# Performance work log

Hardware: AMD Instinct MI355X
Metric: run time of the kernel (lower is better)

Reference implementation:

```python
import jax, jax.numpy as jnp
import numpy as np

N_NODES = 200000
N_EDGES = 600000
FP = 128


def _gru_cell(x, h, wih, whh, bih, bhh):
    # torch.nn.GRUCell: gates ordered (r, z, n)
    gi = x @ wih.T + bih
    gh = h @ whh.T + bhh
    ir, iz, inn = jnp.split(gi, 3, axis=-1)
    hr, hz, hn = jnp.split(gh, 3, axis=-1)
    r = jax.nn.sigmoid(ir + hr)
    z = jax.nn.sigmoid(iz + hz)
    n = jnp.tanh(inn + r * hn)
    return (1.0 - z) * n + z * h


def _layer(x, dst, step, aw, ab, tw, tb, wih, whh, bih, bhh):
    n_nodes = x.shape[0]
    x_i = x[dst]  # [E, F] gather of target-node features
    if step == 0:
        h_s = jnp.broadcast_to(jnp.sum(x_i, axis=-1, keepdims=True), x_i.shape)
    else:
        h_s = x_i
    esv = jax.nn.leaky_relu(jnp.concatenate([h_s, x_i], axis=-1) @ aw.T + ab)  # [E,1]
    asv = jax.nn.softmax(esv, axis=-1)  # size-1 softmax -> ones (faithful)
    cs = jax.nn.elu(asv * (h_s @ tw.T + tb))  # dropout is identity at eval
    m = _gru_cell(cs, h_s, wih, whh, bih, bhh)  # per-edge GRU update [E,F]
    return jax.ops.segment_sum(m, dst, num_segments=n_nodes)  # scatter-add aggregate


def setup_inputs() -> dict:
    key = jax.random.key(0)
    ks = jax.random.split(key, 20)
    s = 1.0 / np.sqrt(FP)
    inp = {
        "x": jax.random.normal(ks[0], (N_NODES, FP), dtype=jnp.float32),
        "edge_index": jax.random.randint(ks[1], (2, N_EDGES), 0, N_NODES, dtype=jnp.int64),
    }
    i = 2
    for l in range(2):
        inp[f"align_w{l}"] = jax.random.uniform(ks[i], (1, 2 * FP), jnp.float32, -s, s); i += 1
        inp[f"align_b{l}"] = jax.random.uniform(ks[i], (1,), jnp.float32, -s, s); i += 1
        inp[f"attend_w{l}"] = jax.random.uniform(ks[i], (FP, FP), jnp.float32, -s, s); i += 1
        inp[f"attend_b{l}"] = jax.random.uniform(ks[i], (FP,), jnp.float32, -s, s); i += 1
        inp[f"wih{l}"] = jax.random.uniform(ks[i], (3 * FP, FP), jnp.float32, -s, s); i += 1
        inp[f"whh{l}"] = jax.random.uniform(ks[i], (3 * FP, FP), jnp.float32, -s, s); i += 1
        inp[f"bih{l}"] = jax.random.uniform(ks[i], (3 * FP,), jnp.float32, -s, s); i += 1
        inp[f"bhh{l}"] = jax.random.uniform(ks[i], (3 * FP,), jnp.float32, -s, s); i += 1
    return inp


def reference(x, edge_index,
              align_w0, align_b0, attend_w0, attend_b0, wih0, whh0, bih0, bhh0,
              align_w1, align_b1, attend_w1, attend_b1, wih1, whh1, bih1, bhh1):
    dst = edge_index[1]
    x = _layer(x, dst, 0, align_w0, align_b0, attend_w0, attend_b0, wih0, whh0, bih0, bhh0)
    x = _layer(x, dst, 1, align_w1, align_b1, attend_w1, attend_b1, wih1, whh1, bih1, bhh1)
    return x
```

## Files before the change

### kernel.cpp

```cpp
#include <hip/hip_runtime.h>
#include <cmath>

#define NN 200000
#define NE 600000

typedef __bf16 bf16x8 __attribute__((ext_vector_type(8)));
typedef float f32x4 __attribute__((ext_vector_type(4)));

#define LOG2E 1.44269504088896340736f
__device__ __forceinline__ float fexp2(float x) { return __builtin_amdgcn_exp2f(x); }
__device__ __forceinline__ float frcp(float x) { return __builtin_amdgcn_rcpf(x); }
__device__ __forceinline__ float sigm(float v) { return frcp(1.0f + fexp2(-LOG2E * v)); }
__device__ __forceinline__ float ftanh(float v) {
  float t = fexp2(-2.0f * LOG2E * fabsf(v));
  float r = (1.0f - t) * frcp(1.0f + t);
  return __builtin_copysignf(r, v);
}
__device__ __forceinline__ float eluf(float v) { return v > 0.0f ? v : fexp2(LOG2E * v) - 1.0f; }

__device__ __forceinline__ unsigned short bfr(float f) {
  unsigned u = __float_as_uint(f);
  u += 0x7FFFu + ((u >> 16) & 1u);
  return (unsigned short)(u >> 16);
}
__device__ __forceinline__ void bsplit(float v, unsigned short& hi, unsigned short& lo) {
  unsigned short h = bfr(v);
  float hf = __uint_as_float(((unsigned)h) << 16);
  hi = h;
  lo = bfr(v - hf);
}


__global__ __launch_bounds__(256) void hist_kernel(const int* __restrict__ dst,
                                                   int* __restrict__ deg) {
  int e = blockIdx.x * 256 + threadIdx.x;
  if (e < NE) atomicAdd(&deg[dst[e]], 1);
}

__global__ __launch_bounds__(512) void prep_kernel(const float* __restrict__ attw0,
                                                   const float* __restrict__ whh0,
                                                   float* __restrict__ rwt0,
                                                   float* __restrict__ rwh0) {
  int t = threadIdx.x;
  if (t < 128) {
    float s = 0.f;
    for (int k = 0; k < 128; k++) s += attw0[t * 128 + k];
    rwt0[t] = s;
  } else {
    int j = t - 128;
    float s = 0.f;
    for (int k = 0; k < 128; k++) s += whh0[j * 128 + k];
    rwh0[j] = s;
  }
}

__global__ __launch_bounds__(256) void pack_kernel(
    const float* __restrict__ wih0, const float* __restrict__ tw1,
    const float* __restrict__ wih1, const float* __restrict__ whh1,
    unsigned short* __restrict__ w0ph, unsigned short* __restrict__ w0pl,
    unsigned short* __restrict__ w1ph, unsigned short* __restrict__ w1pl,
    unsigned short* __restrict__ w2ph, unsigned short* __restrict__ w2pl) {
  int g = blockIdx.x * 256 + threadIdx.x;
  unsigned short *PH, *PL;
  const float* row;
  int l;
  if (g < 6144) { l = g; PH = w0ph; PL = w0pl; }
  else if (g < 8192) { l = g - 6144; PH = w1ph; PL = w1pl; }
  else if (g < 20480) { l = g - 8192; PH = w2ph; PL = w2pl; }
  else return;
  int lane = l & 63, ks = (l >> 6) & 3, nt = l >> 8;
  int n = nt * 16 + (lane & 15);
  int k0 = ks * 32 + (lane >> 4) * 8;
  if (g < 6144) row = wih0 + n * 128;
  else if (g < 8192) row = tw1 + n * 128;
  else row = (n < 384) ? wih1 + n * 128 : whh1 + (n - 384) * 128;
  unsigned uh[4], ul[4];
  for (int p = 0; p < 4; p++) {
    unsigned short ah, al, bh, bl;
    bsplit(row[k0 + 2 * p], ah, al);
    bsplit(row[k0 + 2 * p + 1], bh, bl);
    uh[p] = (unsigned)ah | ((unsigned)bh << 16);
    ul[p] = (unsigned)al | ((unsigned)bl << 16);
  }
  *(uint4*)&PH[l * 8] = make_uint4(uh[0], uh[1], uh[2], uh[3]);
  *(uint4*)&PL[l * 8] = make_uint4(ul[0], ul[1], ul[2], ul[3]);
}

#define MFMA3(accv, ah, al, bh, bl)                                          \
  accv = __builtin_amdgcn_mfma_f32_16x16x32_bf16(ah, bh, accv, 0, 0, 0);     \
  accv = __builtin_amdgcn_mfma_f32_16x16x32_bf16(ah, bl, accv, 0, 0, 0);     \
  accv = __builtin_amdgcn_mfma_f32_16x16x32_bf16(al, bh, accv, 0, 0, 0);

__global__ __launch_bounds__(256, 2) void layer0_kernel(
    const float* __restrict__ x, const float* __restrict__ tb0,
    const unsigned short* __restrict__ w0ph, const unsigned short* __restrict__ w0pl,
    const float* __restrict__ bih0, const float* __restrict__ bhh0,
    const float* __restrict__ rwt0, const float* __restrict__ rwh0,
    const int* __restrict__ deg, float* __restrict__ x1) {
  __shared__ float s_lds[32];
  __shared__ float deg_lds[32];
  __shared__ unsigned short csh[32 * 136];
  __shared__ unsigned short csl[32 * 136];

  const int tid = threadIdx.x;
  const int lane = tid & 63;
  const int wv = tid >> 6;
  const int n0 = blockIdx.x * 32;

  if (tid < 32) deg_lds[tid] = (float)deg[n0 + tid];

  {
    int m = tid >> 3, c = (tid & 7) * 16;
    const float4* xr = (const float4*)(x + (size_t)(n0 + m) * 128 + c);
    float a = 0.f;
#pragma unroll
    for (int q = 0; q < 4; q++) { float4 v = xr[q]; a += v.x + v.y + v.z + v.w; }
#pragma unroll
    for (int o = 1; o < 8; o <<= 1) a += __shfl_xor(a, o, 64);
    if ((tid & 7) == 0) s_lds[m] = a;
  }
  __syncthreads();

  {
    int m = tid >> 3, c0 = (tid & 7) * 16;
    float s = s_lds[m];
#pragma unroll
    for (int q = 0; q < 4; q++) {
      int k = c0 + q * 4;
      unsigned short h0, l0, h1, l1, h2, l2, h3, l3;
      bsplit(eluf(fmaf(s, rwt0[k], tb0[k])), h0, l0);
      bsplit(eluf(fmaf(s, rwt0[k + 1], tb0[k + 1])), h1, l1);
      bsplit(eluf(fmaf(s, rwt0[k + 2], tb0[k + 2])), h2, l2);
      bsplit(eluf(fmaf(s, rwt0[k + 3], tb0[k + 3])), h3, l3);
      *(uint2*)&csh[m * 136 + k] =
          make_uint2((unsigned)h0 | ((unsigned)h1 << 16), (unsigned)h2 | ((unsigned)h3 << 16));
      *(uint2*)&csl[m * 136 + k] =
          make_uint2((unsigned)l0 | ((unsigned)l1 << 16), (unsigned)l2 | ((unsigned)l3 << 16));
    }
  }
  __syncthreads();

  const int mrow = lane & 15;
  const int kq = (lane >> 4) * 8;
  const int quad = lane >> 4;
  f32x4 acc[2][2][3] = {};
#pragma unroll
  for (int ks = 0; ks < 4; ks++) {
    bf16x8 a0h = *(const bf16x8*)&csh[mrow * 136 + ks * 32 + kq];
    bf16x8 a0l = *(const bf16x8*)&csl[mrow * 136 + ks * 32 + kq];
    bf16x8 a1h = *(const bf16x8*)&csh[(16 + mrow) * 136 + ks * 32 + kq];
    bf16x8 a1l = *(const bf16x8*)&csl[(16 + mrow) * 136 + ks * 32 + kq];
#pragma unroll
    for (int jj = 0; jj < 2; jj++) {
      int jt = wv + jj * 4;
#pragma unroll
      for (int g = 0; g < 3; g++) {
        int nt = g * 8 + jt;
        size_t base = (size_t)((nt * 4 + ks) * 64 + lane) * 8;
        bf16x8 bh = *(const bf16x8*)&w0ph[base];
        bf16x8 bl = *(const bf16x8*)&w0pl[base];
        MFMA3(acc[0][jj][g], a0h, a0l, bh, bl);
        MFMA3(acc[1][jj][g], a1h, a1l, bh, bl);
      }
    }
  }

  float bir[2], biz[2], bin_[2], bhr[2], bhz[2], bhn[2], rwr[2], rwz[2], rwn[2];
#pragma unroll
  for (int jj = 0; jj < 2; jj++) {
    int j = (wv + jj * 4) * 16 + mrow;
    bir[jj] = bih0[j]; biz[jj] = bih0[j + 128]; bin_[jj] = bih0[j + 256];
    bhr[jj] = bhh0[j]; bhz[jj] = bhh0[j + 128]; bhn[jj] = bhh0[j + 256];
    rwr[jj] = rwh0[j]; rwz[jj] = rwh0[j + 128]; rwn[jj] = rwh0[j + 256];
  }
#pragma unroll
  for (int mt = 0; mt < 2; mt++) {
#pragma unroll
    for (int reg = 0; reg < 4; reg++) {
      int m = mt * 16 + quad * 4 + reg;
      float s = s_lds[m];
      float dd = deg_lds[m];
#pragma unroll
      for (int jj = 0; jj < 2; jj++) {
        float gir = acc[mt][jj][0][reg] + bir[jj];
        float giz = acc[mt][jj][1][reg] + biz[jj];
        float gin = acc[mt][jj][2][reg] + bin_[jj];
        float ghr = fmaf(s, rwr[jj], bhr[jj]);
        float ghz = fmaf(s, rwz[jj], bhz[jj]);
        float ghn = fmaf(s, rwn[jj], bhn[jj]);
        float r = sigm(gir + ghr);
        float z = sigm(giz + ghz);
        float nn = ftanh(fmaf(r, ghn, gin));
        int j = (wv + jj * 4) * 16 + mrow;
        x1[(size_t)(n0 + m) * 128 + j] = dd * ((1.f - z) * nn + z * s);
      }
    }
  }
}

__global__ __launch_bounds__(256, 2) void layer1_kernel(
    const float* __restrict__ x1, const float* __restrict__ tb1,
    const unsigned short* __restrict__ w1ph, const unsigned short* __restrict__ w1pl,
    const unsigned short* __restrict__ w2ph, const unsigned short* __restrict__ w2pl,
    const float* __restrict__ bih1, const float* __restrict__ bhh1,
    const int* __restrict__ deg, float* __restrict__ out) {
  __shared__ unsigned short hh[32 * 136];
  __shared__ unsigned short hl[32 * 136];
  __shared__ unsigned short ch[32 * 136];
  __shared__ unsigned short cl[32 * 136];
  __shared__ float deg_lds[32];

  const int tid = threadIdx.x;
  const int lane = tid & 63;
  const int wv = tid >> 6;
  const int n0 = blockIdx.x * 32;
  const int mrow = lane & 15;
  const int kq = (lane >> 4) * 8;
  const int quad = lane >> 4;

  if (tid < 32) deg_lds[tid] = (float)deg[n0 + tid];

  {
    int m = tid >> 3, c0 = (tid & 7) * 16;
    const float4* xr = (const float4*)(x1 + (size_t)(n0 + m) * 128 + c0);
#pragma unroll
    for (int q = 0; q < 4; q++) {
      float4 v = xr[q];
      unsigned short h0, l0, h1, l1, h2, l2, h3, l3;
      bsplit(v.x, h0, l0); bsplit(v.y, h1, l1);
      bsplit(v.z, h2, l2); bsplit(v.w, h3, l3);
      *(uint2*)&hh[m * 136 + c0 + q * 4] =
          make_uint2((unsigned)h0 | ((unsigned)h1 << 16), (unsigned)h2 | ((unsigned)h3 << 16));
      *(uint2*)&hl[m * 136 + c0 + q * 4] =
          make_uint2((unsigned)l0 | ((unsigned)l1 << 16), (unsigned)l2 | ((unsigned)l3 << 16));
    }
  }
  __syncthreads();

  f32x4 acc1[2][2] = {};
#pragma unroll
  for (int ks = 0; ks < 4; ks++) {
    bf16x8 a0h = *(const bf16x8*)&hh[mrow * 136 + ks * 32 + kq];
    bf16x8 a0l = *(const bf16x8*)&hl[mrow * 136 + ks * 32 + kq];
    bf16x8 a1h = *(const bf16x8*)&hh[(16 + mrow) * 136 + ks * 32 + kq];
    bf16x8 a1l = *(const bf16x8*)&hl[(16 + mrow) * 136 + ks * 32 + kq];
#pragma unroll
    for (int jj = 0; jj < 2; jj++) {
      int nt = wv + jj * 4;
      size_t base = (size_t)((nt * 4 + ks) * 64 + lane) * 8;
      bf16x8 bh = *(const bf16x8*)&w1ph[base];
      bf16x8 bl = *(const bf16x8*)&w1pl[base];
      MFMA3(acc1[0][jj], a0h, a0l, bh, bl);
      MFMA3(acc1[1][jj], a1h, a1l, bh, bl);
    }
  }
  {
    float tbj[2];
#pragma unroll
    for (int jj = 0; jj < 2; jj++) tbj[jj] = tb1[(wv + jj * 4) * 16 + mrow];
#pragma unroll
    for (int mt = 0; mt < 2; mt++)
#pragma unroll
      for (int jj = 0; jj < 2; jj++)
#pragma unroll
        for (int reg = 0; reg < 4; reg++) {
          int m = mt * 16 + quad * 4 + reg;
          unsigned short vh, vl;
          bsplit(eluf(acc1[mt][jj][reg] + tbj[jj]), vh, vl);
          unsigned pv = (unsigned)vh | ((unsigned)vl << 16);
          unsigned pu = __shfl_xor(pv, 1, 64);
          if ((lane & 1) == 0) {
            int j = (wv + jj * 4) * 16 + mrow;
            unsigned hpack = (pv & 0xFFFFu) | (pu << 16);
            unsigned lpack = (pv >> 16) | (pu & 0xFFFF0000u);
            *(unsigned*)&ch[m * 136 + j] = hpack;
            *(unsigned*)&cl[m * 136 + j] = lpack;
          }
        }
  }
  __syncthreads();

  f32x4 acc2[2][2][6] = {};
#pragma unroll
  for (int ks = 0; ks < 4; ks++) {
    bf16x8 c0h = *(const bf16x8*)&ch[mrow * 136 + ks * 32 + kq];
    bf16x8 c0l = *(const bf16x8*)&cl[mrow * 136 + ks * 32 + kq];
    bf16x8 c1h = *(const bf16x8*)&ch[(16 + mrow) * 136 + ks * 32 + kq];
    bf16x8 c1l = *(const bf16x8*)&cl[(16 + mrow) * 136 + ks * 32 + kq];
    bf16x8 x0h = *(const bf16x8*)&hh[mrow * 136 + ks * 32 + kq];
    bf16x8 x0l = *(const bf16x8*)&hl[mrow * 136 + ks * 32 + kq];
    bf16x8 x1h = *(const bf16x8*)&hh[(16 + mrow) * 136 + ks * 32 + kq];
    bf16x8 x1l = *(const bf16x8*)&hl[(16 + mrow) * 136 + ks * 32 + kq];
#pragma unroll
    for (int jj = 0; jj < 2; jj++) {
      int jt = wv + jj * 4;
#pragma unroll
      for (int g = 0; g < 3; g++) {
        int nt = g * 8 + jt;
        size_t base = (size_t)((nt * 4 + ks) * 64 + lane) * 8;
        bf16x8 bh = *(const bf16x8*)&w2ph[base];
        bf16x8 bl = *(const bf16x8*)&w2pl[base];
        MFMA3(acc2[0][jj][g], c0h, c0l, bh, bl);
        MFMA3(acc2[1][jj][g], c1h, c1l, bh, bl);
      }
#pragma unroll
      for (int g = 0; g < 3; g++) {
        int nt = 24 + g * 8 + jt;
        size_t base = (size_t)((nt * 4 + ks) * 64 + lane) * 8;
        bf16x8 bh = *(const bf16x8*)&w2ph[base];
        bf16x8 bl = *(const bf16x8*)&w2pl[base];
        MFMA3(acc2[0][jj][3 + g], x0h, x0l, bh, bl);
        MFMA3(acc2[1][jj][3 + g], x1h, x1l, bh, bl);
      }
    }
  }

  float bir[2], biz[2], bin_[2], bhr[2], bhz[2], bhn[2];
#pragma unroll
  for (int jj = 0; jj < 2; jj++) {
    int j = (wv + jj * 4) * 16 + mrow;
    bir[jj] = bih1[j]; biz[jj] = bih1[j + 128]; bin_[jj] = bih1[j + 256];
    bhr[jj] = bhh1[j]; bhz[jj] = bhh1[j + 128]; bhn[jj] = bhh1[j + 256];
  }
#pragma unroll
  for (int mt = 0; mt < 2; mt++) {
#pragma unroll
    for (int reg = 0; reg < 4; reg++) {
      int m = mt * 16 + quad * 4 + reg;
      float dd = deg_lds[m];
#pragma unroll
      for (int jj = 0; jj < 2; jj++) {
        int j = (wv + jj * 4) * 16 + mrow;
        float gir = acc2[mt][jj][0][reg] + bir[jj];
        float giz = acc2[mt][jj][1][reg] + biz[jj];
        float gin = acc2[mt][jj][2][reg] + bin_[jj];
        float ghr = acc2[mt][jj][3][reg] + bhr[jj];
        float ghz = acc2[mt][jj][4][reg] + bhz[jj];
        float ghn = acc2[mt][jj][5][reg] + bhn[jj];
        float r = sigm(gir + ghr);
        float z = sigm(giz + ghz);
        float nn = ftanh(fmaf(r, ghn, gin));
        float hfull = (float)(*(const __bf16*)&hh[m * 136 + j]) +
                      (float)(*(const __bf16*)&hl[m * 136 + j]);
        out[(size_t)(n0 + m) * 128 + j] = dd * ((1.f - z) * nn + z * hfull);
      }
    }
  }
}

extern "C" void kernel_launch(void* const* d_in, const int* in_sizes, int n_in,
                              void* d_out, int out_size, void* d_ws, size_t ws_size,
                              hipStream_t stream) {
  const float* x     = (const float*)d_in[0];
  const int*   edge  = (const int*)d_in[1];
  const float* attw0 = (const float*)d_in[4];
  const float* attb0 = (const float*)d_in[5];
  const float* wih0  = (const float*)d_in[6];
  const float* whh0  = (const float*)d_in[7];
  const float* bih0  = (const float*)d_in[8];
  const float* bhh0  = (const float*)d_in[9];
  const float* attw1 = (const float*)d_in[12];
  const float* attb1 = (const float*)d_in[13];
  const float* wih1  = (const float*)d_in[14];
  const float* whh1  = (const float*)d_in[15];
  const float* bih1  = (const float*)d_in[16];
  const float* bhh1  = (const float*)d_in[17];

  float* ws   = (float*)d_ws;
  float* x1   = ws;
  int*   deg  = (int*)(ws + 25600000);
  float* rwt0 = ws + 25800000;
  float* rwh0 = ws + 25800128;
  unsigned short* wp = (unsigned short*)(ws + 25800512);
  unsigned short* w0ph = wp;
  unsigned short* w0pl = wp + 49152;
  unsigned short* w1ph = wp + 98304;
  unsigned short* w1pl = wp + 114688;
  unsigned short* w2ph = wp + 131072;
  unsigned short* w2pl = wp + 229376;

  const int* dst = edge + NE;

  hipMemsetAsync(deg, 0, NN * sizeof(int), stream);
  hist_kernel<<<(NE + 255) / 256, 256, 0, stream>>>(dst, deg);
  prep_kernel<<<1, 512, 0, stream>>>(attw0, whh0, rwt0, rwh0);
  pack_kernel<<<80, 256, 0, stream>>>(wih0, attw1, wih1, whh1,
                                      w0ph, w0pl, w1ph, w1pl, w2ph, w2pl);
  layer0_kernel<<<NN / 32, 256, 0, stream>>>(x, attb0, w0ph, w0pl, bih0, bhh0,
                                             rwt0, rwh0, deg, x1);
  layer1_kernel<<<NN / 32, 256, 0, stream>>>(x1, attb1, w1ph, w1pl, w2ph, w2pl,
                                             bih1, bhh1, deg, (float*)d_out);
}
```

Before: 493.7 us.

## Use 64-node tiles with 8 waves each owning one output column tile

Both layer kernels now process 64 nodes per block with 512 threads. Each of the 8 waves owns a single 16-column output tile across four 16-row M tiles, so each weight fragment loaded from global is reused across four MFMA row tiles instead of two. Layer1 also interleaves the x-side GRU matmul with the attend matmul in the first K loop. It moves its LDS buffers to dynamic shared memory with a raised size limit. The cost is more accumulator registers per thread (24 f32x4 in layer1) and larger LDS use, which may lower occupancy.

```diff
diff --git a/kernel.cpp b/kernel.cpp
--- a/kernel.cpp
+++ b/kernel.cpp
@@ -91,23 +91,23 @@
   accv = __builtin_amdgcn_mfma_f32_16x16x32_bf16(ah, bl, accv, 0, 0, 0);     \
   accv = __builtin_amdgcn_mfma_f32_16x16x32_bf16(al, bh, accv, 0, 0, 0);
 
-__global__ __launch_bounds__(256, 2) void layer0_kernel(
+__global__ __launch_bounds__(512, 4) void layer0_kernel(
     const float* __restrict__ x, const float* __restrict__ tb0,
     const unsigned short* __restrict__ w0ph, const unsigned short* __restrict__ w0pl,
     const float* __restrict__ bih0, const float* __restrict__ bhh0,
     const float* __restrict__ rwt0, const float* __restrict__ rwh0,
     const int* __restrict__ deg, float* __restrict__ x1) {
-  __shared__ float s_lds[32];
-  __shared__ float deg_lds[32];
-  __shared__ unsigned short csh[32 * 136];
-  __shared__ unsigned short csl[32 * 136];
+  __shared__ float s_lds[64];
+  __shared__ float deg_lds[64];
+  __shared__ unsigned short csh[64 * 136];
+  __shared__ unsigned short csl[64 * 136];
 
   const int tid = threadIdx.x;
   const int lane = tid & 63;
   const int wv = tid >> 6;
-  const int n0 = blockIdx.x * 32;
-
-  if (tid < 32) deg_lds[tid] = (float)deg[n0 + tid];
+  const int n0 = blockIdx.x * 64;
+
+  if (tid < 64) deg_lds[tid] = (float)deg[n0 + tid];
 
   {
     int m = tid >> 3, c = (tid & 7) * 16;
@@ -143,82 +143,73 @@
   const int mrow = lane & 15;
   const int kq = (lane >> 4) * 8;
   const int quad = lane >> 4;
-  f32x4 acc[2][2][3] = {};
+  f32x4 acc[4][3] = {};
 #pragma unroll
   for (int ks = 0; ks < 4; ks++) {
-    bf16x8 a0h = *(const bf16x8*)&csh[mrow * 136 + ks * 32 + kq];
-    bf16x8 a0l = *(const bf16x8*)&csl[mrow * 136 + ks * 32 + kq];
-    bf16x8 a1h = *(const bf16x8*)&csh[(16 + mrow) * 136 + ks * 32 + kq];
-    bf16x8 a1l = *(const bf16x8*)&csl[(16 + mrow) * 136 + ks * 32 + kq];
-#pragma unroll
-    for (int jj = 0; jj < 2; jj++) {
-      int jt = wv + jj * 4;
-#pragma unroll
-      for (int g = 0; g < 3; g++) {
-        int nt = g * 8 + jt;
-        size_t base = (size_t)((nt * 4 + ks) * 64 + lane) * 8;
-        bf16x8 bh = *(const bf16x8*)&w0ph[base];
-        bf16x8 bl = *(const bf16x8*)&w0pl[base];
-        MFMA3(acc[0][jj][g], a0h, a0l, bh, bl);
-        MFMA3(acc[1][jj][g], a1h, a1l, bh, bl);
-      }
-    }
-  }
-
-  float bir[2], biz[2], bin_[2], bhr[2], bhz[2], bhn[2], rwr[2], rwz[2], rwn[2];
-#pragma unroll
-  for (int jj = 0; jj < 2; jj++) {
-    int j = (wv + jj * 4) * 16 + mrow;
-    bir[jj] = bih0[j]; biz[jj] = bih0[j + 128]; bin_[jj] = bih0[j + 256];
-    bhr[jj] = bhh0[j]; bhz[jj] = bhh0[j + 128]; bhn[jj] = bhh0[j + 256];
-    rwr[jj] = rwh0[j]; rwz[jj] = rwh0[j + 128]; rwn[jj] = rwh0[j + 256];
-  }
-#pragma unroll
-  for (int mt = 0; mt < 2; mt++) {
+    bf16x8 ah[4], al[4];
+#pragma unroll
+    for (int mt = 0; mt < 4; mt++) {
+      ah[mt] = *(const bf16x8*)&csh[(mt * 16 + mrow) * 136 + ks * 32 + kq];
+      al[mt] = *(const bf16x8*)&csl[(mt * 16 + mrow) * 136 + ks * 32 + kq];
+    }
+#pragma unroll
+    for (int g = 0; g < 3; g++) {
+      int nt = g * 8 + wv;
+      size_t base = (size_t)((nt * 4 + ks) * 64 + lane) * 8;
+      bf16x8 bh = *(const bf16x8*)&w0ph[base];
+      bf16x8 bl = *(const bf16x8*)&w0pl[base];
+#pragma unroll
+      for (int mt = 0; mt < 4; mt++) { MFMA3(acc[mt][g], ah[mt], al[mt], bh, bl); }
+    }
+  }
+
+  const int j = wv * 16 + mrow;
+  float bir = bih0[j], biz = bih0[j + 128], bin_ = bih0[j + 256];
+  float bhr = bhh0[j], bhz = bhh0[j + 128], bhn = bhh0[j + 256];
+  float rwr = rwh0[j], rwz = rwh0[j + 128], rwn = rwh0[j + 256];
+#pragma unroll
+  for (int mt = 0; mt < 4; mt++) {
 #pragma unroll
     for (int reg = 0; reg < 4; reg++) {
       int m = mt * 16 + quad * 4 + reg;
       float s = s_lds[m];
       float dd = deg_lds[m];
-#pragma unroll
-      for (int jj = 0; jj < 2; jj++) {
-        float gir = acc[mt][jj][0][reg] + bir[jj];
-        float giz = acc[mt][jj][1][reg] + biz[jj];
-        float gin = acc[mt][jj][2][reg] + bin_[jj];
-        float ghr = fmaf(s, rwr[jj], bhr[jj]);
-        float ghz = fmaf(s, rwz[jj], bhz[jj]);
-        float ghn = fmaf(s, rwn[jj], bhn[jj]);
-        float r = sigm(gir + ghr);
-        float z = sigm(giz + ghz);
-        float nn = ftanh(fmaf(r, ghn, gin));
-        int j = (wv + jj * 4) * 16 + mrow;
-        x1[(size_t)(n0 + m) * 128 + j] = dd * ((1.f - z) * nn + z * s);
-      }
-    }
-  }
-}
-
-__global__ __launch_bounds__(256, 2) void layer1_kernel(
+      float gir = acc[mt][0][reg] + bir;
+      float giz = acc[mt][1][reg] + biz;
+      float gin = acc[mt][2][reg] + bin_;
+      float ghr = fmaf(s, rwr, bhr);
+      float ghz = fmaf(s, rwz, bhz);
+      float ghn = fmaf(s, rwn, bhn);
+      float r = sigm(gir + ghr);
+      float z = sigm(giz + ghz);
+      float nn2 = ftanh(fmaf(r, ghn, gin));
+      x1[(size_t)(n0 + m) * 128 + j] = dd * ((1.f - z) * nn2 + z * s);
+    }
+  }
+}
+
+__global__ __launch_bounds__(512, 2) void layer1_kernel(
     const float* __restrict__ x1, const float* __restrict__ tb1,
     const unsigned short* __restrict__ w1ph, const unsigned short* __restrict__ w1pl,
     const unsigned short* __restrict__ w2ph, const unsigned short* __restrict__ w2pl,
     const float* __restrict__ bih1, const float* __restrict__ bhh1,
     const int* __restrict__ deg, float* __restrict__ out) {
-  __shared__ unsigned short hh[32 * 136];
-  __shared__ unsigned short hl[32 * 136];
-  __shared__ unsigned short ch[32 * 136];
-  __shared__ unsigned short cl[32 * 136];
-  __shared__ float deg_lds[32];
+  extern __shared__ unsigned short smem[];
+  unsigned short* hh = smem;
+  unsigned short* hl = smem + 8704;
+  unsigned short* ch = smem + 17408;
+  unsigned short* cl = smem + 26112;
+  __shared__ float deg_lds[64];
 
   const int tid = threadIdx.x;
   const int lane = tid & 63;
   const int wv = tid >> 6;
-  const int n0 = blockIdx.x * 32;
+  const int n0 = blockIdx.x * 64;
   const int mrow = lane & 15;
   const int kq = (lane >> 4) * 8;
   const int quad = lane >> 4;
 
-  if (tid < 32) deg_lds[tid] = (float)deg[n0 + tid];
+  if (tid < 64) deg_lds[tid] = (float)deg[n0 + tid];
 
   {
     int m = tid >> 3, c0 = (tid & 7) * 16;
@@ -237,113 +228,97 @@
   }
   __syncthreads();
 
-  f32x4 acc1[2][2] = {};
+  f32x4 acc1[4] = {};
+  f32x4 acc2[4][6] = {};
 #pragma unroll
   for (int ks = 0; ks < 4; ks++) {
-    bf16x8 a0h = *(const bf16x8*)&hh[mrow * 136 + ks * 32 + kq];
-    bf16x8 a0l = *(const bf16x8*)&hl[mrow * 136 + ks * 32 + kq];
-    bf16x8 a1h = *(const bf16x8*)&hh[(16 + mrow) * 136 + ks * 32 + kq];
-    bf16x8 a1l = *(const bf16x8*)&hl[(16 + mrow) * 136 + ks * 32 + kq];
-#pragma unroll
-    for (int jj = 0; jj < 2; jj++) {
-      int nt = wv + jj * 4;
-      size_t base = (size_t)((nt * 4 + ks) * 64 + lane) * 8;
+    bf16x8 xh[4], xl[4];
+#pragma unroll
+    for (int mt = 0; mt < 4; mt++) {
+      xh[mt] = *(const bf16x8*)&hh[(mt * 16 + mrow) * 136 + ks * 32 + kq];
+      xl[mt] = *(const bf16x8*)&hl[(mt * 16 + mrow) * 136 + ks * 32 + kq];
+    }
+    {
+      size_t base = (size_t)((wv * 4 + ks) * 64 + lane) * 8;
       bf16x8 bh = *(const bf16x8*)&w1ph[base];
       bf16x8 bl = *(const bf16x8*)&w1pl[base];
-      MFMA3(acc1[0][jj], a0h, a0l, bh, bl);
-      MFMA3(acc1[1][jj], a1h, a1l, bh, bl);
-    }
-  }
+#pragma unroll
+      for (int mt = 0; mt < 4; mt++) { MFMA3(acc1[mt], xh[mt], xl[mt], bh, bl); }
+    }
+#pragma unroll
+    for (int g = 0; g < 3; g++) {
+      int nt = 24 + g * 8 + wv;
+      size_t base = (size_t)((nt * 4 + ks) * 64 + lane) * 8;
+      bf16x8 bh = *(const bf16x8*)&w2ph[base];
+      bf16x8 bl = *(const bf16x8*)&w2pl[base];
+#pragma unroll
+      for (int mt = 0; mt < 4; mt++) { MFMA3(acc2[mt][3 + g], xh[mt], xl[mt], bh, bl); }
+    }
+  }
+
   {
-    float tbj[2];
-#pragma unroll
-    for (int jj = 0; jj < 2; jj++) tbj[jj] = tb1[(wv + jj * 4) * 16 + mrow];
-#pragma unroll
-    for (int mt = 0; mt < 2; mt++)
-#pragma unroll
-      for (int jj = 0; jj < 2; jj++)
-#pragma unroll
-        for (int reg = 0; reg < 4; reg++) {
-          int m = mt * 16 + quad * 4 + reg;
-          unsigned short vh, vl;
-          bsplit(eluf(acc1[mt][jj][reg] + tbj[jj]), vh, vl);
-          unsigned pv = (unsigned)vh | ((unsigned)vl << 16);
-          unsigned pu = __shfl_xor(pv, 1, 64);
-          if ((lane & 1) == 0) {
-            int j = (wv + jj * 4) * 16 + mrow;
-            unsigned hpack = (pv & 0xFFFFu) | (pu << 16);
-            unsigned lpack = (pv >> 16) | (pu & 0xFFFF0000u);
-            *(unsigned*)&ch[m * 136 + j] = hpack;
-            *(unsigned*)&cl[m * 136 + j] = lpack;
-          }
+    float tbj = tb1[wv * 16 + mrow];
+#pragma unroll
+    for (int mt = 0; mt < 4; mt++) {
+#pragma unroll
+      for (int reg = 0; reg < 4; reg++) {
+        int m = mt * 16 + quad * 4 + reg;
+        unsigned short vh, vl;
+        bsplit(eluf(acc1[mt][reg] + tbj), vh, vl);
+        unsigned pv = (unsigned)vh | ((unsigned)vl << 16);
+        unsigned pu = __shfl_xor(pv, 1, 64);
+        if ((lane & 1) == 0) {
+          int jc = wv * 16 + mrow;
+          unsigned hpack = (pv & 0xFFFFu) | (pu << 16);
+          unsigned lpack = (pv >> 16) | (pu & 0xFFFF0000u);
+          *(unsigned*)&ch[m * 136 + jc] = hpack;
+          *(unsigned*)&cl[m * 136 + jc] = lpack;
         }
+      }
+    }
   }
   __syncthreads();
 
-  f32x4 acc2[2][2][6] = {};
 #pragma unroll
   for (int ks = 0; ks < 4; ks++) {
-    bf16x8 c0h = *(const bf16x8*)&ch[mrow * 136 + ks * 32 + kq];
-    bf16x8 c0l = *(const bf16x8*)&cl[mrow * 136 + ks * 32 + kq];
-    bf16x8 c1h = *(const bf16x8*)&ch[(16 + mrow) * 136 + ks * 32 + kq];
-    bf16x8 c1l = *(const bf16x8*)&cl[(16 + mrow) * 136 + ks * 32 + kq];
-    bf16x8 x0h = *(const bf16x8*)&hh[mrow * 136 + ks * 32 + kq];
-    bf16x8 x0l = *(const bf16x8*)&hl[mrow * 136 + ks * 32 + kq];
-    bf16x8 x1h = *(const bf16x8*)&hh[(16 + mrow) * 136 + ks * 32 + kq];
-    bf16x8 x1l = *(const bf16x8*)&hl[(16 + mrow) * 136 + ks * 32 + kq];
-#pragma unroll
-    for (int jj = 0; jj < 2; jj++) {
-      int jt = wv + jj * 4;
-#pragma unroll
-      for (int g = 0; g < 3; g++) {
-        int nt = g * 8 + jt;
-        size_t base = (size_t)((nt * 4 + ks) * 64 + lane) * 8;
-        bf16x8 bh = *(const bf16x8*)&w2ph[base];
-        bf16x8 bl = *(const bf16x8*)&w2pl[base];
-        MFMA3(acc2[0][jj][g], c0h, c0l, bh, bl);
-        MFMA3(acc2[1][jj][g], c1h, c1l, bh, bl);
-      }
-#pragma unroll
-      for (int g = 0; g < 3; g++) {
-        int nt = 24 + g * 8 + jt;
-        size_t base = (size_t)((nt * 4 + ks) * 64 + lane) * 8;
-        bf16x8 bh = *(const bf16x8*)&w2ph[base];
-        bf16x8 bl = *(const bf16x8*)&w2pl[base];
-        MFMA3(acc2[0][jj][3 + g], x0h, x0l, bh, bl);
-        MFMA3(acc2[1][jj][3 + g], x1h, x1l, bh, bl);
-      }
-    }
-  }
-
-  float bir[2], biz[2], bin_[2], bhr[2], bhz[2], bhn[2];
-#pragma unroll
-  for (int jj = 0; jj < 2; jj++) {
-    int j = (wv + jj * 4) * 16 + mrow;
-    bir[jj] = bih1[j]; biz[jj] = bih1[j + 128]; bin_[jj] = bih1[j + 256];
-    bhr[jj] = bhh1[j]; bhz[jj] = bhh1[j + 128]; bhn[jj] = bhh1[j + 256];
-  }
-#pragma unroll
-  for (int mt = 0; mt < 2; mt++) {
+    bf16x8 ah[4], al[4];
+#pragma unroll
+    for (int mt = 0; mt < 4; mt++) {
+      ah[mt] = *(const bf16x8*)&ch[(mt * 16 + mrow) * 136 + ks * 32 + kq];
+      al[mt] = *(const bf16x8*)&cl[(mt * 16 + mrow) * 136 + ks * 32 + kq];
+    }
+#pragma unroll
+    for (int g = 0; g < 3; g++) {
+      int nt = g * 8 + wv;
+      size_t base = (size_t)((nt * 4 + ks) * 64 + lane) * 8;
+      bf16x8 bh = *(const bf16x8*)&w2ph[base];
+      bf16x8 bl = *(const bf16x8*)&w2pl[base];
+#pragma unroll
+      for (int mt = 0; mt < 4; mt++) { MFMA3(acc2[mt][g], ah[mt], al[mt], bh, bl); }
+    }
+  }
+
+  const int j = wv * 16 + mrow;
+  float bir = bih1[j], biz = bih1[j + 128], bin_ = bih1[j + 256];
+  float bhr = bhh1[j], bhz = bhh1[j + 128], bhn = bhh1[j + 256];
+#pragma unroll
+  for (int mt = 0; mt < 4; mt++) {
 #pragma unroll
     for (int reg = 0; reg < 4; reg++) {
       int m = mt * 16 + quad * 4 + reg;
       float dd = deg_lds[m];
-#pragma unroll
-      for (int jj = 0; jj < 2; jj++) {
-        int j = (wv + jj * 4) * 16 + mrow;
-        float gir = acc2[mt][jj][0][reg] + bir[jj];
-        float giz = acc2[mt][jj][1][reg] + biz[jj];
-        float gin = acc2[mt][jj][2][reg] + bin_[jj];
-        float ghr = acc2[mt][jj][3][reg] + bhr[jj];
-        float ghz = acc2[mt][jj][4][reg] + bhz[jj];
-        float ghn = acc2[mt][jj][5][reg] + bhn[jj];
-        float r = sigm(gir + ghr);
-        float z = sigm(giz + ghz);
-        float nn = ftanh(fmaf(r, ghn, gin));
-        float hfull = (float)(*(const __bf16*)&hh[m * 136 + j]) +
-                      (float)(*(const __bf16*)&hl[m * 136 + j]);
-        out[(size_t)(n0 + m) * 128 + j] = dd * ((1.f - z) * nn + z * hfull);
-      }
+      float gir = acc2[mt][0][reg] + bir;
+      float giz = acc2[mt][1][reg] + biz;
+      float gin = acc2[mt][2][reg] + bin_;
+      float ghr = acc2[mt][3][reg] + bhr;
+      float ghz = acc2[mt][4][reg] + bhz;
+      float ghn = acc2[mt][5][reg] + bhn;
+      float r = sigm(gir + ghr);
+      float z = sigm(giz + ghz);
+      float nn2 = ftanh(fmaf(r, ghn, gin));
+      float hfull = (float)(*(const __bf16*)&hh[m * 136 + j]) +
+                    (float)(*(const __bf16*)&hl[m * 136 + j]);
+      out[(size_t)(n0 + m) * 128 + j] = dd * ((1.f - z) * nn2 + z * hfull);
     }
   }
 }
@@ -381,13 +356,20 @@
 
   const int* dst = edge + NE;
 
+  static bool attr_done = false;
+  if (!attr_done) {
+    hipFuncSetAttribute(reinterpret_cast<const void*>(layer1_kernel),
+                        hipFuncAttributeMaxDynamicSharedMemorySize, 69632);
+    attr_done = true;
+  }
+
   hipMemsetAsync(deg, 0, NN * sizeof(int), stream);
   hist_kernel<<<(NE + 255) / 256, 256, 0, stream>>>(dst, deg);
   prep_kernel<<<1, 512, 0, stream>>>(attw0, whh0, rwt0, rwh0);
   pack_kernel<<<80, 256, 0, stream>>>(wih0, attw1, wih1, whh1,
                                       w0ph, w0pl, w1ph, w1pl, w2ph, w2pl);
-  layer0_kernel<<<NN / 32, 256, 0, stream>>>(x, attb0, w0ph, w0pl, bih0, bhh0,
+  layer0_kernel<<<NN / 64, 512, 0, stream>>>(x, attb0, w0ph, w0pl, bih0, bhh0,
                                              rwt0, rwh0, deg, x1);
-  layer1_kernel<<<NN / 32, 256, 0, stream>>>(x1, attb1, w1ph, w1pl, w2ph, w2pl,
-                                             bih1, bhh1, deg, (float*)d_out);
-}
+  layer1_kernel<<<NN / 64, 512, 69632, stream>>>(x1, attb1, w1ph, w1pl, w2ph, w2pl,
+                                                 bih1, bhh1, deg, (float*)d_out);
+}
```

Measured after the change: 450.1 us. 1.1x faster.
